# Performance work log

Hardware: AMD Instinct MI355X
Metric: run time of the kernel (lower is better)

Reference implementation:

```python
import jax, jax.numpy as jnp
import numpy as np


def _dwconv(x, w, b):
    # depthwise conv, NCHW, kernel [C,1,k,k], SAME padding k//2
    k = w.shape[-1]
    p = k // 2
    out = jax.lax.conv_general_dilated(x, w, (1, 1), [(p, p), (p, p)],
                                       feature_group_count=x.shape[1])
    return out + b[None, :, None, None]


def _conv1x1(x, W, b):
    return jnp.einsum('oc,bchw->bohw', W, x) + b[None, :, None, None]


def _ca_weight(q, k):
    # q,k: [b,c,h,w] -> energy [b,h,w,h+w]
    eH = jnp.einsum('bchw,bcgw->bhwg', q, k)  # attend along H (column)
    eW = jnp.einsum('bchw,bchv->bhwv', q, k)  # attend along W (row)
    return jnp.concatenate([eH, eW], axis=3)


def _ca_map(att, v):
    # att: [b,h,w,h+w], v: [b,c,h,w]
    h = v.shape[2]
    outH = jnp.einsum('bcgw,bhwg->bchw', v, att[..., :h])
    outW = jnp.einsum('bchv,bhwv->bchw', v, att[..., h:])
    return outH + outW


def _cc_block(cnn, Wq, bq, Wk, bk, Wv, bv, gamma):
    q = _conv1x1(cnn, Wq, bq)
    k = _conv1x1(cnn, Wk, bk)
    v = _conv1x1(cnn, Wv, bv)
    att = jax.nn.softmax(_ca_weight(q, k), axis=1)  # softmax over H axis, as in torch F.softmax(energy, 1)
    return gamma * _ca_map(att, v) + cnn


def _ppeg(x, w7, b7, w5, b5, w3, b3, H, W):
    C = x.shape[1]
    cnn = x.T.reshape(1, C, H, W)
    out = _dwconv(cnn, w7, b7) + cnn + _dwconv(cnn, w5, b5) + _dwconv(cnn, w3, b3)
    return out.reshape(C, H * W).T  # [N, C]


def setup_inputs() -> dict:
    key = jax.random.key(0)
    N, DIM, HID, QK = 65536, 1024, 512, 64  # N = 256^2
    ks = jax.random.split(key, 26)
    s = 0.02
    inp = {
        'h0': jax.random.normal(ks[0], (N, DIM), jnp.float32),
        'w7': jax.random.normal(ks[1], (DIM, 1, 7, 7)) * s,
        'b7': jax.random.normal(ks[2], (DIM,)) * s,
        'w5': jax.random.normal(ks[3], (DIM, 1, 5, 5)) * s,
        'b5': jax.random.normal(ks[4], (DIM,)) * s,
        'w3': jax.random.normal(ks[5], (DIM, 1, 3, 3)) * s,
        'b3': jax.random.normal(ks[6], (DIM,)) * s,
        'W1': jax.random.normal(ks[7], (HID, DIM)) * s,
        'b1': jax.random.normal(ks[8], (HID,)) * s,
        'Wq': jax.random.normal(ks[9], (QK, HID)) * s,
        'bq': jax.random.normal(ks[10], (QK,)) * s,
        'Wk': jax.random.normal(ks[11], (QK, HID)) * s,
        'bk': jax.random.normal(ks[12], (QK,)) * s,
        'Wv': jax.random.normal(ks[13], (HID, HID)) * s,
        'bv': jax.random.normal(ks[14], (HID,)) * s,
        'gamma': jax.random.normal(ks[15], ()) * 0.5,
        'Wq1': jax.random.normal(ks[16], (QK, HID)) * s,
        'bq1': jax.random.normal(ks[17], (QK,)) * s,
        'Wk1': jax.random.normal(ks[18], (QK, HID)) * s,
        'bk1': jax.random.normal(ks[19], (QK,)) * s,
        'Wv1': jax.random.normal(ks[20], (HID, HID)) * s,
        'bv1': jax.random.normal(ks[21], (HID,)) * s,
        'gamma1': jax.random.normal(ks[22], ()) * 0.5,
        'Wfc': jax.random.normal(ks[23], (1, HID)) * s,
        'bfc': jax.random.normal(ks[24], (1,)) * s,
    }
    return inp


def reference(h0, w7, b7, w5, b5, w3, b3, W1, b1,
              Wq, bq, Wk, bk, Wv, bv, gamma,
              Wq1, bq1, Wk1, bk1, Wv1, bv1, gamma1, Wfc, bfc):
    N = h0.shape[0]
    side = int(np.ceil(np.sqrt(N)))
    pad = side * side - N
    h1 = jnp.concatenate([h0, h0[:pad]], axis=0) if pad > 0 else h0
    # PPEG positional encoding (multi-kernel depthwise conv)
    h1 = _ppeg(h1, w7, b7, w5, b5, w3, b3, side, side)
    # fc1: Linear(1024->512) + ReLU  (h1 already square -> second pad is no-op)
    h2 = jax.nn.relu(h1 @ W1.T + b1)  # [N, 512]
    # CCAttention (two criss-cross blocks + fc to 1 logit)
    cnn = h2.T.reshape(1, h2.shape[1], side, side)
    out = _cc_block(cnn, Wq, bq, Wk, bk, Wv, bv, gamma)
    out1 = _cc_block(out, Wq1, bq1, Wk1, bk1, Wv1, bv1, gamma1)
    out1 = out1.reshape(out1.shape[1], side * side).T  # [N, 512]
    logits = out1 @ Wfc.T + bfc  # [N, 1]
    A = jax.nn.softmax(logits.T, axis=1)  # [1, N] attention over instances
    return A
```

## Files before the change

kernel.cpp:

```cpp
#include <hip/hip_runtime.h>

#define HW 65536
#define SIDE 256

typedef __attribute__((ext_vector_type(8))) short short8v;
typedef __attribute__((ext_vector_type(4))) float f32x4;

__device__ __forceinline__ ushort f2bf(float f) {
  unsigned int u = __builtin_bit_cast(unsigned int, f);
  u = (u + 0x7fff + ((u >> 16) & 1)) >> 16;
  return (ushort)u;
}
__device__ __forceinline__ float bf2f(unsigned int u) {
  return __builtin_bit_cast(float, (u & 0xffffu) << 16);
}
__device__ __forceinline__ void gld16(const void* g, void* l) {
  __builtin_amdgcn_global_load_lds(
      (const __attribute__((address_space(1))) void*)g,
      (__attribute__((address_space(3))) void*)l, 16, 0, 0);
}

__global__ __launch_bounds__(256) void k_transpose_nc(const float* __restrict__ in,
                                                      ushort* __restrict__ out) {
  __shared__ float t[32][33];
  const int n0 = blockIdx.x << 5, c0 = blockIdx.y << 5;
  const int tx = threadIdx.x, ty = threadIdx.y;
#pragma unroll
  for (int r = 0; r < 32; r += 8)
    t[ty + r][tx] = in[(size_t)(n0 + ty + r) * 1024 + c0 + tx];
  __syncthreads();
#pragma unroll
  for (int r = 0; r < 32; r += 8)
    out[(size_t)(c0 + ty + r) * HW + n0 + tx] = f2bf(t[tx][ty + r]);
}

__global__ __launch_bounds__(256) void k_wcomb(const float* __restrict__ w7,
    const float* __restrict__ b7, const float* __restrict__ w5,
    const float* __restrict__ b5, const float* __restrict__ w3,
    const float* __restrict__ b3, float* __restrict__ wc, float* __restrict__ bc) {
  const int c = blockIdx.x * 256 + threadIdx.x;
  if (c >= 1024) return;
  float w[49];
#pragma unroll
  for (int i = 0; i < 49; i++) w[i] = w7[c * 49 + i];
  for (int dy = 0; dy < 5; dy++)
    for (int dx = 0; dx < 5; dx++)
      w[(dy + 1) * 7 + (dx + 1)] += w5[c * 25 + dy * 5 + dx];
  for (int dy = 0; dy < 3; dy++)
    for (int dx = 0; dx < 3; dx++)
      w[(dy + 2) * 7 + (dx + 2)] += w3[c * 9 + dy * 3 + dx];
  w[3 * 7 + 3] += 1.0f;
#pragma unroll
  for (int i = 0; i < 49; i++) wc[c * 49 + i] = w[i];
  bc[c] = b7[c] + b5[c] + b3[c];
}

__global__ __launch_bounds__(256) void k_dwconv7(const ushort* __restrict__ X,
    const float* __restrict__ wc, const float* __restrict__ bc,
    ushort* __restrict__ out) {
  __shared__ float tile[38][264];
  const int c = blockIdx.y;
  const int y0 = blockIdx.x << 5;
  const int tid = threadIdx.x;
  const ushort* Xc = X + (size_t)c * HW;

  float w[49];
#pragma unroll
  for (int i = 0; i < 49; i++) w[i] = wc[c * 49 + i];
  const float bcv = bc[c];

  for (int i = tid; i < 38 * 8; i += 256) {
    const int r = i >> 3, cc = i & 7;
    tile[r][cc < 4 ? cc : 256 + cc] = 0.f;
  }
  for (int i = tid; i < 38 * 64; i += 256) {
    const int r = i >> 6, j4 = i & 63;
    const int y = y0 - 3 + r;
    float4 f = {0.f, 0.f, 0.f, 0.f};
    if (y >= 0 && y < SIDE) {
      const uint2 u = *(const uint2*)(Xc + y * SIDE + (j4 << 2));
      f.x = bf2f(u.x); f.y = bf2f(u.x >> 16);
      f.z = bf2f(u.y); f.w = bf2f(u.y >> 16);
    }
    *(float4*)&tile[r][(j4 << 2) + 4] = f;
  }
  __syncthreads();

  const int lx = (tid & 63) << 2;
  const int ry = (tid >> 6) << 3;
  float acc[8][4] = {};
#pragma unroll
  for (int r = 0; r < 14; r++) {
    float rv[12];
    *(float4*)&rv[0] = *(const float4*)&tile[ry + r][lx];
    *(float4*)&rv[4] = *(const float4*)&tile[ry + r][lx + 4];
    *(float4*)&rv[8] = *(const float4*)&tile[ry + r][lx + 8];
#pragma unroll
    for (int m = 0; m < 8; m++) {
      const int dy = r - m;
      if (dy < 0 || dy > 6) continue;
#pragma unroll
      for (int dx = 0; dx < 7; dx++) {
        const float ww = w[dy * 7 + dx];
#pragma unroll
        for (int o = 0; o < 4; o++) acc[m][o] += ww * rv[o + 1 + dx];
      }
    }
  }
#pragma unroll
  for (int m = 0; m < 8; m++) {
    ushort4 o4 = {f2bf(acc[m][0] + bcv), f2bf(acc[m][1] + bcv),
                  f2bf(acc[m][2] + bcv), f2bf(acc[m][3] + bcv)};
    *(ushort4*)&out[(size_t)c * HW + (y0 + ry + m) * SIDE + lx] = o4;
  }
}

__global__ __launch_bounds__(256) void k_tr_u16(const ushort* __restrict__ in,
    ushort* __restrict__ out, int R, int C, long long bs) {
  __shared__ ushort t[64][66];
  const size_t base = (size_t)blockIdx.z * bs;
  const int c0 = blockIdx.x << 6, r0 = blockIdx.y << 6;
  const int tx = threadIdx.x & 63, ty = threadIdx.x >> 6;
#pragma unroll
  for (int i = 0; i < 64; i += 4)
    t[ty + i][tx] = in[base + (size_t)(r0 + ty + i) * C + c0 + tx];
  __syncthreads();
#pragma unroll
  for (int i = 0; i < 64; i += 4)
    out[base + (size_t)(c0 + ty + i) * R + r0 + tx] = t[tx][ty + i];
}

template <int BN, int BIAS, int RELU, int OUTF, int OUTB>
__global__ __launch_bounds__(256) void k_mm(
    const ushort* __restrict__ A, int lda, long long bsA,
    const ushort* __restrict__ B, int ldb, long long bsB,
    const float* __restrict__ bias,
    float* __restrict__ Cf, ushort* __restrict__ Cb, int ldc, long long bsC,
    int K) {
  static_assert(BN == 64 || BN == 128, "BN");
  constexpr int FN = BN / 32;
  __shared__ __align__(16) ushort As[128 * 32];
  __shared__ __align__(16) ushort Bs[BN * 32];
  const int tid = threadIdx.x;
  const int bm = blockIdx.x << 7, bn = blockIdx.y * BN;
  const long long zA = (long long)blockIdx.z * bsA;
  const long long zB = (long long)blockIdx.z * bsB;
  const long long zC = (long long)blockIdx.z * bsC;

  const int sr = tid >> 2, sq = tid & 3;
  const int sw0 = (sr >> 1) & 3;
  const int sw1 = ((sr + 64) >> 1) & 3;
  const ushort* Ap0 = A + zA + (size_t)(bm + sr) * lda + ((sq ^ sw0) << 3);
  const ushort* Ap1 = A + zA + (size_t)(bm + sr + 64) * lda + ((sq ^ sw1) << 3);
  const ushort* Bp0 = B + zB + (size_t)(bn + sr) * ldb + ((sq ^ sw0) << 3);
  const ushort* Bp1 = nullptr;
  if constexpr (BN == 128)
    Bp1 = B + zB + (size_t)(bn + sr + 64) * ldb + ((sq ^ sw1) << 3);
  ushort* wA0 = &As[sr * 32 + sq * 8];
  ushort* wA1 = &As[(sr + 64) * 32 + sq * 8];
  ushort* wB0 = &Bs[sr * 32 + sq * 8];
  ushort* wB1 = nullptr;
  if constexpr (BN == 128) wB1 = &Bs[(sr + 64) * 32 + sq * 8];

  const int lane = tid & 63, wv = tid >> 6;
  const int wm = wv & 1, wn = wv >> 1;
  const int fr = lane & 15, kq = lane >> 4;
  int offA[4], offB[FN];
#pragma unroll
  for (int mi = 0; mi < 4; mi++) {
    const int row = wm * 64 + mi * 16 + fr;
    offA[mi] = row * 32 + ((kq ^ ((row >> 1) & 3)) << 3);
  }
#pragma unroll
  for (int ni = 0; ni < FN; ni++) {
    const int row = wn * (BN / 2) + ni * 16 + fr;
    offB[ni] = row * 32 + ((kq ^ ((row >> 1) & 3)) << 3);
  }

  f32x4 acc[4][FN];
#pragma unroll
  for (int mi = 0; mi < 4; mi++)
#pragma unroll
    for (int ni = 0; ni < FN; ni++) acc[mi][ni] = (f32x4){0.f, 0.f, 0.f, 0.f};

  for (int k0 = 0; k0 < K; k0 += 32) {
    __syncthreads();
    gld16(Ap0 + k0, wA0);
    gld16(Ap1 + k0, wA1);
    gld16(Bp0 + k0, wB0);
    if constexpr (BN == 128) gld16(Bp1 + k0, wB1);
    __syncthreads();
    short8v a[4], b[FN];
#pragma unroll
    for (int mi = 0; mi < 4; mi++) a[mi] = *(const short8v*)&As[offA[mi]];
#pragma unroll
    for (int ni = 0; ni < FN; ni++) b[ni] = *(const short8v*)&Bs[offB[ni]];
#pragma unroll
    for (int mi = 0; mi < 4; mi++)
#pragma unroll
      for (int ni = 0; ni < FN; ni++)
        acc[mi][ni] = __builtin_amdgcn_mfma_f32_16x16x32_bf16(a[mi], b[ni], acc[mi][ni], 0, 0, 0);
  }

#pragma unroll
  for (int mi = 0; mi < 4; mi++) {
#pragma unroll
    for (int ni = 0; ni < FN; ni++) {
#pragma unroll
      for (int r = 0; r < 4; r++) {
        const int row = bm + wm * 64 + mi * 16 + (lane >> 4) * 4 + r;
        const int col = bn + wn * (BN / 2) + ni * 16 + fr;
        float v = acc[mi][ni][r];
        if (BIAS == 1) v += bias[row];
        if (BIAS == 2) v += bias[col];
        if (RELU) v = fmaxf(v, 0.f);
        const size_t idx = (size_t)(zC + (size_t)row * ldc + col);
        if (OUTF) Cf[idx] = v;
        if (OUTB) Cb[idx] = f2bf(v);
      }
    }
  }
}

__global__ __launch_bounds__(256) void k_softmax_bf16(const ushort* __restrict__ E,
    ushort* __restrict__ Att, int outerStride, int hStride) {
  const size_t base = (size_t)blockIdx.x * outerStride + threadIdx.x;
  float m = -3.4e38f, s = 0.f;
  for (int h = 0; h < 256; h++) {
    const float x = bf2f(E[base + (size_t)h * hStride]);
    const float nm = fmaxf(m, x);
    s = s * __expf(m - nm) + __expf(x - nm);
    m = nm;
  }
  const float inv = 1.0f / s;
  for (int h = 0; h < 256; h++) {
    const size_t i = base + (size_t)h * hStride;
    Att[i] = f2bf(__expf(bf2f(E[i]) - m) * inv);
  }
}

__global__ __launch_bounds__(256) void k_merge2(const ushort* __restrict__ O,
    const ushort* __restrict__ TH, const ushort* __restrict__ CN,
    const float* __restrict__ gammap, ushort* __restrict__ outB) {
  __shared__ ushort t[32][34];
  const float g = *gammap;
  const size_t base = (size_t)blockIdx.z * HW;
  const int h0 = blockIdx.y << 5, w0 = blockIdx.x << 5;
  const int tx = threadIdx.x, ty = threadIdx.y;
#pragma unroll
  for (int r = 0; r < 32; r += 8)
    t[ty + r][tx] = TH[base + (w0 + ty + r) * SIDE + h0 + tx];
  __syncthreads();
#pragma unroll
  for (int r = 0; r < 32; r += 8) {
    const size_t idx = base + (h0 + ty + r) * SIDE + w0 + tx;
    const float v = g * (bf2f(O[idx]) + bf2f(t[tx][ty + r])) + bf2f(CN[idx]);
    outB[idx] = f2bf(v);
  }
}

__global__ __launch_bounds__(256) void k_logits(const ushort* __restrict__ X,
    const float* __restrict__ Wfc, const float* __restrict__ bfc,
    float* __restrict__ L) {
  const int n = blockIdx.x * 256 + threadIdx.x;
  float s = 0.f;
  for (int j = 0; j < 512; j++) s += bf2f(X[(size_t)j * HW + n]) * Wfc[j];
  L[n] = s + bfc[0];
}

__global__ __launch_bounds__(256) void k_smax_reduce(const float* __restrict__ L,
                                                     float* __restrict__ red) {
  __shared__ float sm[256];
  const int tid = threadIdx.x;
  float m = -3.4e38f;
  for (int i = tid; i < HW; i += 256) m = fmaxf(m, L[i]);
  sm[tid] = m;
  __syncthreads();
  for (int s = 128; s > 0; s >>= 1) {
    if (tid < s) sm[tid] = fmaxf(sm[tid], sm[tid + s]);
    __syncthreads();
  }
  const float M = sm[0];
  __syncthreads();
  float sum = 0.f;
  for (int i = tid; i < HW; i += 256) sum += expf(L[i] - M);
  sm[tid] = sum;
  __syncthreads();
  for (int s = 128; s > 0; s >>= 1) {
    if (tid < s) sm[tid] += sm[tid + s];
    __syncthreads();
  }
  if (tid == 0) { red[0] = M; red[1] = sm[0]; }
}

__global__ __launch_bounds__(256) void k_smax_write(const float* __restrict__ L,
    const float* __restrict__ red, float* __restrict__ out) {
  const int n = blockIdx.x * 256 + threadIdx.x;
  out[n] = expf(L[n] - red[0]) * (1.0f / red[1]);
}

__global__ void k_f2b(const float* __restrict__ in, ushort* __restrict__ out, int n) {
  const int i = blockIdx.x * 256 + threadIdx.x;
  if (i < n) out[i] = f2bf(in[i]);
}

__global__ void k_cpy(const float* __restrict__ a, float* __restrict__ b, int n) {
  const int i = blockIdx.x * 256 + threadIdx.x;
  if (i < n) b[i] = a[i];
}

extern "C" void kernel_launch(void* const* d_in, const int* in_sizes, int n_in,
                              void* d_out, int out_size, void* d_ws, size_t ws_size,
                              hipStream_t stream) {
  const float* h0 = (const float*)d_in[0];
  const float* w7 = (const float*)d_in[1];
  const float* b7 = (const float*)d_in[2];
  const float* w5 = (const float*)d_in[3];
  const float* b5 = (const float*)d_in[4];
  const float* w3 = (const float*)d_in[5];
  const float* b3 = (const float*)d_in[6];
  const float* W1 = (const float*)d_in[7];
  const float* b1 = (const float*)d_in[8];
  const float* Wq = (const float*)d_in[9];
  const float* bq = (const float*)d_in[10];
  const float* Wk = (const float*)d_in[11];
  const float* bk = (const float*)d_in[12];
  const float* Wv = (const float*)d_in[13];
  const float* bv = (const float*)d_in[14];
  const float* gamma = (const float*)d_in[15];
  const float* Wq1 = (const float*)d_in[16];
  const float* bq1 = (const float*)d_in[17];
  const float* Wk1 = (const float*)d_in[18];
  const float* bk1 = (const float*)d_in[19];
  const float* Wv1 = (const float*)d_in[20];
  const float* bv1 = (const float*)d_in[21];
  const float* gamma1 = (const float*)d_in[22];
  const float* Wfc = (const float*)d_in[23];
  const float* bfc = (const float*)d_in[24];

  char* W = (char*)d_ws;
  const size_t MB = 1 << 20;
  ushort* Xb    = (ushort*)(W + 0);
  ushort* H2b   = (ushort*)(W + 0);
  ushort* H2t   = (ushort*)(W + 64 * MB);
  ushort* qkt   = (ushort*)(W + 128 * MB);
  ushort* AttW  = (ushort*)(W + 144 * MB);
  ushort* AttH  = (ushort*)(W + 176 * MB);
  ushort* H1b   = (ushort*)(W + 256 * MB);
  ushort* H1t   = (ushort*)(W + 384 * MB);
  ushort* Vb    = (ushort*)(W + 384 * MB);
  ushort* vTb   = (ushort*)(W + 448 * MB);
  ushort* Ob    = (ushort*)(W + 512 * MB);
  ushort* THbb  = (ushort*)(W + 576 * MB);
  ushort* Eb    = (ushort*)(W + 640 * MB);
  ushort* W1b   = (ushort*)(W + 704 * MB);
  ushort* Wvb   = (ushort*)(W + 705 * MB);
  ushort* Wv1b  = (ushort*)(W + 705 * MB + 512 * 1024);
  ushort* Wqkb  = (ushort*)(W + 706 * MB);
  ushort* Wqk1b = (ushort*)(W + 706 * MB + 128 * 1024);
  float*  wcomb = (float*)(W + 706 * MB + 256 * 1024);
  float*  bcomb = (float*)(W + 706 * MB + 464 * 1024);
  float*  bqk   = (float*)(W + 706 * MB + 472 * 1024);
  float*  bqk1  = (float*)(W + 706 * MB + 474 * 1024);
  float*  L     = (float*)(W + 707 * MB);
  float*  red   = (float*)(W + 707 * MB + 256 * 1024);

  k_f2b<<<2048, 256, 0, stream>>>(W1, W1b, 512 * 1024);
  k_f2b<<<1024, 256, 0, stream>>>(Wv, Wvb, 256 * 1024);
  k_f2b<<<1024, 256, 0, stream>>>(Wv1, Wv1b, 256 * 1024);
  k_f2b<<<128, 256, 0, stream>>>(Wq, Wqkb, 32768);
  k_f2b<<<128, 256, 0, stream>>>(Wk, Wqkb + 32768, 32768);
  k_f2b<<<128, 256, 0, stream>>>(Wq1, Wqk1b, 32768);
  k_f2b<<<128, 256, 0, stream>>>(Wk1, Wqk1b + 32768, 32768);
  k_cpy<<<1, 256, 0, stream>>>(bq, bqk, 64);
  k_cpy<<<1, 256, 0, stream>>>(bk, bqk + 64, 64);
  k_cpy<<<1, 256, 0, stream>>>(bq1, bqk1, 64);
  k_cpy<<<1, 256, 0, stream>>>(bk1, bqk1 + 64, 64);
  k_wcomb<<<4, 256, 0, stream>>>(w7, b7, w5, b5, w3, b3, wcomb, bcomb);

  k_transpose_nc<<<dim3(2048, 32), dim3(32, 8), 0, stream>>>(h0, Xb);
  k_dwconv7<<<dim3(8, 1024), 256, 0, stream>>>(Xb, wcomb, bcomb, H1b);
  k_tr_u16<<<dim3(1024, 16, 1), 256, 0, stream>>>(H1b, H1t, 1024, HW, 0);

  k_mm<128, 1, 1, 0, 1><<<dim3(4, 512, 1), 256, 0, stream>>>(
      W1b, 1024, 0, H1t, 1024, 0, b1, nullptr, H2b, HW, 0, 1024);
  k_tr_u16<<<dim3(1024, 8, 1), 256, 0, stream>>>(H2b, H2t, 512, HW, 0);

  auto cc_block = [&](const ushort* act, ushort* cnn, const ushort* Wqk_,
                      const float* bqk_, const ushort* Wv_, const float* bv_,
                      const float* gam) {
    k_mm<128, 2, 0, 0, 1><<<dim3(512, 1, 1), 256, 0, stream>>>(
        act, 512, 0, Wqk_, 512, 0, bqk_, nullptr, qkt, 128, 0, 512);
    k_mm<128, 1, 0, 0, 1><<<dim3(4, 512, 1), 256, 0, stream>>>(
        Wv_, 512, 0, act, 512, 0, bv_, nullptr, Vb, HW, 0, 512);
    k_tr_u16<<<dim3(4, 4, 512), 256, 0, stream>>>(Vb, vTb, 256, 256, 65536);
    k_mm<128, 0, 0, 0, 1><<<dim3(2, 2, 256), 256, 0, stream>>>(
        qkt, 128, 32768, qkt + 64, 128, 32768, nullptr, nullptr, Eb, 256, 65536, 64);
    k_softmax_bf16<<<256, 256, 0, stream>>>(Eb, AttW, 256, HW);
    k_mm<128, 0, 0, 0, 1><<<dim3(4, 2, 256), 256, 0, stream>>>(
        Vb, HW, 256, AttW, 256, 65536, nullptr, nullptr, Ob, HW, 256, 256);
    k_mm<128, 0, 0, 0, 1><<<dim3(2, 2, 256), 256, 0, stream>>>(
        qkt, 32768, 128, qkt + 64, 32768, 128, nullptr, nullptr, Eb, 256, 65536, 64);
    k_softmax_bf16<<<256, 256, 0, stream>>>(Eb, AttH, HW, 256);
    k_mm<128, 0, 0, 0, 1><<<dim3(4, 2, 256), 256, 0, stream>>>(
        vTb, HW, 256, AttH, 256, 65536, nullptr, nullptr, THbb, HW, 256, 256);
    k_merge2<<<dim3(8, 8, 512), dim3(32, 8), 0, stream>>>(
        Ob, THbb, cnn, gam, cnn);
  };

  cc_block(H2t, H2b, Wqkb, bqk, Wvb, bv, gamma);
  k_tr_u16<<<dim3(1024, 8, 1), 256, 0, stream>>>(H2b, H2t, 512, HW, 0);
  cc_block(H2t, H2b, Wqk1b, bqk1, Wv1b, bv1, gamma1);

  k_logits<<<256, 256, 0, stream>>>(H2b, Wfc, bfc, L);
  k_smax_reduce<<<1, 256, 0, stream>>>(L, red);
  k_smax_write<<<256, 256, 0, stream>>>(L, red, (float*)d_out);
}
```

Baseline: 1.401 ms.

## Fuse weight prep kernels, vectorize MFMA epilogue stores, float4 dwconv tile

Merges the twelve small weight-conversion, bias-copy and filter-combination launches into one prep kernel to cut launch overhead. Swaps the MFMA operand order so each lane holds four consecutive output columns, which lets the GEMM epilogue write float4/ushort4 stores instead of scalar ones. Also retypes the dwconv shared tile as float4 with one-element padding. The operand swap depends on the kq/fr index mapping being consistent with the transposed accumulator layout, and the float4 bias load assumes aligned bias pointers.

```diff
diff --git a/kernel.cpp b/kernel.cpp
--- a/kernel.cpp
+++ b/kernel.cpp
@@ -34,31 +34,58 @@
     out[(size_t)(c0 + ty + r) * HW + n0 + tx] = f2bf(t[tx][ty + r]);
 }
 
-__global__ __launch_bounds__(256) void k_wcomb(const float* __restrict__ w7,
+__global__ __launch_bounds__(256) void k_prep(
+    const float* __restrict__ W1, const float* __restrict__ Wv,
+    const float* __restrict__ Wv1, const float* __restrict__ Wq,
+    const float* __restrict__ Wk, const float* __restrict__ Wq1,
+    const float* __restrict__ Wk1, const float* __restrict__ bq,
+    const float* __restrict__ bk, const float* __restrict__ bq1,
+    const float* __restrict__ bk1, const float* __restrict__ w7,
     const float* __restrict__ b7, const float* __restrict__ w5,
     const float* __restrict__ b5, const float* __restrict__ w3,
-    const float* __restrict__ b3, float* __restrict__ wc, float* __restrict__ bc) {
-  const int c = blockIdx.x * 256 + threadIdx.x;
-  if (c >= 1024) return;
-  float w[49];
-#pragma unroll
-  for (int i = 0; i < 49; i++) w[i] = w7[c * 49 + i];
-  for (int dy = 0; dy < 5; dy++)
-    for (int dx = 0; dx < 5; dx++)
-      w[(dy + 1) * 7 + (dx + 1)] += w5[c * 25 + dy * 5 + dx];
-  for (int dy = 0; dy < 3; dy++)
-    for (int dx = 0; dx < 3; dx++)
-      w[(dy + 2) * 7 + (dx + 2)] += w3[c * 9 + dy * 3 + dx];
-  w[3 * 7 + 3] += 1.0f;
-#pragma unroll
-  for (int i = 0; i < 49; i++) wc[c * 49 + i] = w[i];
-  bc[c] = b7[c] + b5[c] + b3[c];
+    const float* __restrict__ b3,
+    ushort* __restrict__ W1b, ushort* __restrict__ Wvb,
+    ushort* __restrict__ Wv1b, ushort* __restrict__ Wqkb,
+    ushort* __restrict__ Wqk1b, float* __restrict__ bqk,
+    float* __restrict__ bqk1, float* __restrict__ wc, float* __restrict__ bc) {
+  const int i = blockIdx.x * 256 + threadIdx.x;
+  if (i < 524288) { W1b[i] = f2bf(W1[i]); return; }
+  if (i < 786432) { int j = i - 524288; Wvb[j] = f2bf(Wv[j]); return; }
+  if (i < 1048576) { int j = i - 786432; Wv1b[j] = f2bf(Wv1[j]); return; }
+  if (i < 1081344) { int j = i - 1048576; Wqkb[j] = f2bf(Wq[j]); return; }
+  if (i < 1114112) { int j = i - 1081344; Wqkb[32768 + j] = f2bf(Wk[j]); return; }
+  if (i < 1146880) { int j = i - 1114112; Wqk1b[j] = f2bf(Wq1[j]); return; }
+  if (i < 1179648) { int j = i - 1146880; Wqk1b[32768 + j] = f2bf(Wk1[j]); return; }
+  if (i < 1179904) {
+    int j = i - 1179648;
+    if (j < 64) bqk[j] = bq[j];
+    else if (j < 128) bqk[j] = bk[j - 64];
+    else if (j < 192) bqk1[j - 128] = bq1[j - 128];
+    else bqk1[j - 128] = bk1[j - 192];
+    return;
+  }
+  if (i < 1180928) {
+    const int c = i - 1179904;
+    float w[49];
+#pragma unroll
+    for (int t = 0; t < 49; t++) w[t] = w7[c * 49 + t];
+    for (int dy = 0; dy < 5; dy++)
+      for (int dx = 0; dx < 5; dx++)
+        w[(dy + 1) * 7 + (dx + 1)] += w5[c * 25 + dy * 5 + dx];
+    for (int dy = 0; dy < 3; dy++)
+      for (int dx = 0; dx < 3; dx++)
+        w[(dy + 2) * 7 + (dx + 2)] += w3[c * 9 + dy * 3 + dx];
+    w[3 * 7 + 3] += 1.0f;
+#pragma unroll
+    for (int t = 0; t < 49; t++) wc[c * 49 + t] = w[t];
+    bc[c] = b7[c] + b5[c] + b3[c];
+  }
 }
 
 __global__ __launch_bounds__(256) void k_dwconv7(const ushort* __restrict__ X,
     const float* __restrict__ wc, const float* __restrict__ bc,
     ushort* __restrict__ out) {
-  __shared__ float tile[38][264];
+  __shared__ float4 tile4[38][66];
   const int c = blockIdx.y;
   const int y0 = blockIdx.x << 5;
   const int tid = threadIdx.x;
@@ -69,10 +96,8 @@
   for (int i = 0; i < 49; i++) w[i] = wc[c * 49 + i];
   const float bcv = bc[c];
 
-  for (int i = tid; i < 38 * 8; i += 256) {
-    const int r = i >> 3, cc = i & 7;
-    tile[r][cc < 4 ? cc : 256 + cc] = 0.f;
-  }
+  for (int i = tid; i < 38 * 2; i += 256)
+    tile4[i >> 1][(i & 1) ? 65 : 0] = (float4){0.f, 0.f, 0.f, 0.f};
   for (int i = tid; i < 38 * 64; i += 256) {
     const int r = i >> 6, j4 = i & 63;
     const int y = y0 - 3 + r;
@@ -82,19 +107,22 @@
       f.x = bf2f(u.x); f.y = bf2f(u.x >> 16);
       f.z = bf2f(u.y); f.w = bf2f(u.y >> 16);
     }
-    *(float4*)&tile[r][(j4 << 2) + 4] = f;
-  }
-  __syncthreads();
-
-  const int lx = (tid & 63) << 2;
+    tile4[r][j4 + 1] = f;
+  }
+  __syncthreads();
+
+  const int t0 = tid & 63;
   const int ry = (tid >> 6) << 3;
   float acc[8][4] = {};
 #pragma unroll
   for (int r = 0; r < 14; r++) {
     float rv[12];
-    *(float4*)&rv[0] = *(const float4*)&tile[ry + r][lx];
-    *(float4*)&rv[4] = *(const float4*)&tile[ry + r][lx + 4];
-    *(float4*)&rv[8] = *(const float4*)&tile[ry + r][lx + 8];
+    const float4 q0 = tile4[ry + r][t0];
+    const float4 q1 = tile4[ry + r][t0 + 1];
+    const float4 q2 = tile4[ry + r][t0 + 2];
+    rv[0] = q0.x; rv[1] = q0.y; rv[2] = q0.z; rv[3] = q0.w;
+    rv[4] = q1.x; rv[5] = q1.y; rv[6] = q1.z; rv[7] = q1.w;
+    rv[8] = q2.x; rv[9] = q2.y; rv[10] = q2.z; rv[11] = q2.w;
 #pragma unroll
     for (int m = 0; m < 8; m++) {
       const int dy = r - m;
@@ -111,7 +139,7 @@
   for (int m = 0; m < 8; m++) {
     ushort4 o4 = {f2bf(acc[m][0] + bcv), f2bf(acc[m][1] + bcv),
                   f2bf(acc[m][2] + bcv), f2bf(acc[m][3] + bcv)};
-    *(ushort4*)&out[(size_t)c * HW + (y0 + ry + m) * SIDE + lx] = o4;
+    *(ushort4*)&out[(size_t)c * HW + (y0 + ry + m) * SIDE + (t0 << 2)] = o4;
   }
 }
 
@@ -199,24 +227,33 @@
     for (int mi = 0; mi < 4; mi++)
 #pragma unroll
       for (int ni = 0; ni < FN; ni++)
-        acc[mi][ni] = __builtin_amdgcn_mfma_f32_16x16x32_bf16(a[mi], b[ni], acc[mi][ni], 0, 0, 0);
+        acc[mi][ni] = __builtin_amdgcn_mfma_f32_16x16x32_bf16(b[ni], a[mi], acc[mi][ni], 0, 0, 0);
   }
 
 #pragma unroll
   for (int mi = 0; mi < 4; mi++) {
+    const int row = bm + wm * 64 + mi * 16 + fr;
+    const float bs1 = (BIAS == 1) ? bias[row] : 0.f;
 #pragma unroll
     for (int ni = 0; ni < FN; ni++) {
-#pragma unroll
-      for (int r = 0; r < 4; r++) {
-        const int row = bm + wm * 64 + mi * 16 + (lane >> 4) * 4 + r;
-        const int col = bn + wn * (BN / 2) + ni * 16 + fr;
-        float v = acc[mi][ni][r];
-        if (BIAS == 1) v += bias[row];
-        if (BIAS == 2) v += bias[col];
-        if (RELU) v = fmaxf(v, 0.f);
-        const size_t idx = (size_t)(zC + (size_t)row * ldc + col);
-        if (OUTF) Cf[idx] = v;
-        if (OUTB) Cb[idx] = f2bf(v);
+      const int col = bn + wn * (BN / 2) + ni * 16 + (kq << 2);
+      float4 v;
+      v.x = acc[mi][ni][0]; v.y = acc[mi][ni][1];
+      v.z = acc[mi][ni][2]; v.w = acc[mi][ni][3];
+      if (BIAS == 1) { v.x += bs1; v.y += bs1; v.z += bs1; v.w += bs1; }
+      if (BIAS == 2) {
+        const float4 bc4 = *(const float4*)&bias[col];
+        v.x += bc4.x; v.y += bc4.y; v.z += bc4.z; v.w += bc4.w;
+      }
+      if (RELU) {
+        v.x = fmaxf(v.x, 0.f); v.y = fmaxf(v.y, 0.f);
+        v.z = fmaxf(v.z, 0.f); v.w = fmaxf(v.w, 0.f);
+      }
+      const size_t idx = (size_t)(zC + (size_t)row * ldc + col);
+      if (OUTF) *(float4*)&Cf[idx] = v;
+      if (OUTB) {
+        ushort4 u = {f2bf(v.x), f2bf(v.y), f2bf(v.z), f2bf(v.w)};
+        *(ushort4*)&Cb[idx] = u;
       }
     }
   }
@@ -297,16 +334,6 @@
     const float* __restrict__ red, float* __restrict__ out) {
   const int n = blockIdx.x * 256 + threadIdx.x;
   out[n] = expf(L[n] - red[0]) * (1.0f / red[1]);
-}
-
-__global__ void k_f2b(const float* __restrict__ in, ushort* __restrict__ out, int n) {
-  const int i = blockIdx.x * 256 + threadIdx.x;
-  if (i < n) out[i] = f2bf(in[i]);
-}
-
-__global__ void k_cpy(const float* __restrict__ a, float* __restrict__ b, int n) {
-  const int i = blockIdx.x * 256 + threadIdx.x;
-  if (i < n) b[i] = a[i];
 }
 
 extern "C" void kernel_launch(void* const* d_in, const int* in_sizes, int n_in,
@@ -365,18 +392,10 @@
   float*  L     = (float*)(W + 707 * MB);
   float*  red   = (float*)(W + 707 * MB + 256 * 1024);
 
-  k_f2b<<<2048, 256, 0, stream>>>(W1, W1b, 512 * 1024);
-  k_f2b<<<1024, 256, 0, stream>>>(Wv, Wvb, 256 * 1024);
-  k_f2b<<<1024, 256, 0, stream>>>(Wv1, Wv1b, 256 * 1024);
-  k_f2b<<<128, 256, 0, stream>>>(Wq, Wqkb, 32768);
-  k_f2b<<<128, 256, 0, stream>>>(Wk, Wqkb + 32768, 32768);
-  k_f2b<<<128, 256, 0, stream>>>(Wq1, Wqk1b, 32768);
-  k_f2b<<<128, 256, 0, stream>>>(Wk1, Wqk1b + 32768, 32768);
-  k_cpy<<<1, 256, 0, stream>>>(bq, bqk, 64);
-  k_cpy<<<1, 256, 0, stream>>>(bk, bqk + 64, 64);
-  k_cpy<<<1, 256, 0, stream>>>(bq1, bqk1, 64);
-  k_cpy<<<1, 256, 0, stream>>>(bk1, bqk1 + 64, 64);
-  k_wcomb<<<4, 256, 0, stream>>>(w7, b7, w5, b5, w3, b3, wcomb, bcomb);
+  k_prep<<<4613, 256, 0, stream>>>(W1, Wv, Wv1, Wq, Wk, Wq1, Wk1,
+                                   bq, bk, bq1, bk1, w7, b7, w5, b5, w3, b3,
+                                   W1b, Wvb, Wv1b, Wqkb, Wqk1b, bqk, bqk1,
+                                   wcomb, bcomb);
 
   k_transpose_nc<<<dim3(2048, 32), dim3(32, 8), 0, stream>>>(h0, Xb);
   k_dwconv7<<<dim3(8, 1024), 256, 0, stream>>>(Xb, wcomb, bcomb, H1b);
```

Result: no change. 1.421 ms (+1.4%).
